# Performance work log

Hardware: AMD Instinct MI355X
Metric: run time of the kernel (lower is better)

The kernel has to match this reference:

```python
import jax, jax.numpy as jnp
import numpy as np
from math import sqrt

N_IN = 1024
N_OUT = 1024
DEPTH = 10
N_NODES = 2 ** (DEPTH + 1) - 1  # 2047
BATCH = 32768


def setup_inputs() -> dict:
    key = jax.random.key(0)
    k1, k2, k3 = jax.random.split(key, 3)
    f1 = 1.0 / sqrt(N_IN)
    f2 = 1.0 / sqrt(DEPTH + 1)
    x = jax.random.normal(k1, (BATCH, N_IN), dtype=jnp.float32)
    w1s = jax.random.uniform(k2, (N_NODES, N_IN), dtype=jnp.float32, minval=-f1, maxval=f1)
    w2s = jax.random.uniform(k3, (N_NODES, N_OUT), dtype=jnp.float32, minval=-f2, maxval=f2)
    return {"x": x, "w1s": w1s, "w2s": w2s, "depth": DEPTH}


def reference(x, w1s, w2s, depth):
    batch = x.shape[0]

    def step(current_node, _):
        # current_node: [b] int32 node index at this tree level
        plane_score = jnp.einsum('bi,bi->b', x, w1s[current_node])  # [b]
        plane_choice = (plane_score > 0).astype(jnp.int32)
        next_node = current_node * 2 + plane_choice + 1
        return next_node, (current_node, plane_score)

    node0 = jnp.zeros((batch,), dtype=jnp.int32)
    _, (all_nodes, all_scores) = jax.lax.scan(step, node0, None, length=depth + 1)
    all_nodes = all_nodes.T    # [b, depth+1]
    all_scores = all_scores.T  # [b, depth+1]

    selected_w2s = w2s[all_nodes]  # [b, depth+1, nOut]
    y = jnp.einsum('bij,bi->bj', selected_w2s, all_scores)
    return y
```

## Files before the change

### kernel.cpp

```cpp
#include <hip/hip_runtime.h>


typedef float        f32x4 __attribute__((ext_vector_type(4)));
typedef unsigned int u32x4 __attribute__((ext_vector_type(4)));

#define FFF_BATCH  32768
#define FFF_NIN    1024
#define FFF_NOUT   1024
#define FFF_LEVELS 11
#define FFF_NODES  2047
#define FFF_EPS    0.02f

__device__ __forceinline__ f32x4 ld_nt4f(const f32x4* p) { return __builtin_nontemporal_load(p); }
__device__ __forceinline__ float ub(unsigned d, int k) {
    return (float)((d >> (8 * k)) & 0xffu);
}

__global__ void fff_quant_u8(const float* __restrict__ w1, const float* __restrict__ w2,
                             unsigned char* __restrict__ q1, unsigned char* __restrict__ q2,
                             float* __restrict__ s1, float* __restrict__ s2)
{
    const int node = blockIdx.x;
    const int t    = threadIdx.x;
    const int wave = t >> 6;
    const int lane = t & 63;

    const f32x4* r1 = reinterpret_cast<const f32x4*>(w1 + (size_t)node * FFF_NIN);
    const f32x4* r2 = reinterpret_cast<const f32x4*>(w2 + (size_t)node * FFF_NOUT);
    const int si = 64 * (t & 3) + (t >> 2);
    const f32x4 v1 = r1[si];
    const f32x4 v2 = r2[si];

    float m1 = 0.f, m2 = 0.f;
#pragma unroll
    for (int k = 0; k < 4; ++k) {
        m1 = fmaxf(m1, fabsf(v1[k]));
        m2 = fmaxf(m2, fabsf(v2[k]));
    }
#pragma unroll
    for (int m = 1; m < 64; m <<= 1) {
        m1 = fmaxf(m1, __shfl_xor(m1, m, 64));
        m2 = fmaxf(m2, __shfl_xor(m2, m, 64));
    }
    __shared__ float sm1[4], sm2[4];
    if (lane == 0) { sm1[wave] = m1; sm2[wave] = m2; }
    __syncthreads();
    m1 = fmaxf(fmaxf(sm1[0], sm1[1]), fmaxf(sm1[2], sm1[3]));
    m2 = fmaxf(fmaxf(sm2[0], sm2[1]), fmaxf(sm2[2], sm2[3]));

    const float st1 = (m1 > 0.f) ? m1 / 127.f : 1.f;
    const float st2 = (m2 > 0.f) ? m2 / 127.f : 1.f;
    if (t == 0) { s1[node] = st1; s2[node] = st2; }

    unsigned d1 = 0, d2 = 0;
#pragma unroll
    for (int k = 0; k < 4; ++k) {
        const int u1 = (int)rintf(v1[k] / st1) + 128;
        const int u2 = (int)rintf(v2[k] / st2) + 128;
        d1 |= ((unsigned)u1 & 0xffu) << (8 * k);
        d2 |= ((unsigned)u2 & 0xffu) << (8 * k);
    }
    reinterpret_cast<unsigned*>(q1)[(size_t)node * 256 + t] = d1;
    reinterpret_cast<unsigned*>(q2)[(size_t)node * 256 + t] = d2;
}

__global__ __launch_bounds__(256, 4) void fff_main_u8(
    const float*         __restrict__ x,
    const unsigned char* __restrict__ q1,
    const float*         __restrict__ s1,
    const float*         __restrict__ w1f,
    const unsigned char* __restrict__ q2,
    const float*         __restrict__ s2,
    float*               __restrict__ y)
{
    const int row  = blockIdx.x * 4 + (threadIdx.x >> 6);
    const int lane = threadIdx.x & 63;

    const f32x4* x4 = reinterpret_cast<const f32x4*>(x + (size_t)row * FFF_NIN);
    f32x4 xv[4];
#pragma unroll
    for (int c = 0; c < 4; ++c) xv[c] = ld_nt4f(&x4[c * 64 + lane]);

    float sumx = 0.f;
#pragma unroll
    for (int c = 0; c < 4; ++c) {
        sumx += xv[c][0]; sumx += xv[c][1]; sumx += xv[c][2]; sumx += xv[c][3];
    }
#pragma unroll
    for (int m = 1; m < 64; m <<= 1) sumx += __shfl_xor(sumx, m, 64);

    f32x4 acc[4];
#pragma unroll
    for (int c = 0; c < 4; ++c) acc[c] = (f32x4)(0.f);
    float corr = 0.f;

    int node = 0;

#pragma unroll 1
    for (int l = 0; l < FFF_LEVELS; ++l) {
        const int un = __builtin_amdgcn_readfirstlane(node);

        const u32x4 d1 = *reinterpret_cast<const u32x4*>(q1 + (size_t)un * 1024 + lane * 16);
        const u32x4 d2 = *reinterpret_cast<const u32x4*>(q2 + (size_t)un * 1024 + lane * 16);
        const float sc1 = s1[un];
        const float sc2 = s2[un];

        float pu = 0.f;
#pragma unroll
        for (int c = 0; c < 4; ++c) {
#pragma unroll
            for (int k = 0; k < 4; ++k)
                pu = fmaf(xv[c][k], ub(d1[c], k), pu);
        }
#pragma unroll
        for (int m = 1; m < 64; m <<= 1) pu += __shfl_xor(pu, m, 64);

        float p = (pu - 128.f * sumx) * sc1;

        if (__builtin_expect(fabsf(p) < FFF_EPS, 0)) {
            const f32x4* w14 = reinterpret_cast<const f32x4*>(w1f + (size_t)un * FFF_NIN);
            float s = 0.f;
#pragma unroll
            for (int c = 0; c < 4; ++c) {
                const f32x4 w = w14[c * 64 + lane];
                s = fmaf(xv[c][0], w[0], s);
                s = fmaf(xv[c][1], w[1], s);
                s = fmaf(xv[c][2], w[2], s);
                s = fmaf(xv[c][3], w[3], s);
            }
#pragma unroll
            for (int m = 1; m < 64; m <<= 1) s += __shfl_xor(s, m, 64);
            p = s;
        }

        const float s2l = p * sc2;
        corr = fmaf(s2l, 128.f, corr);
#pragma unroll
        for (int c = 0; c < 4; ++c) {
#pragma unroll
            for (int k = 0; k < 4; ++k)
                acc[c][k] = fmaf(s2l, ub(d2[c], k), acc[c][k]);
        }

        node = node * 2 + 1 + ((p > 0.f) ? 1 : 0);
    }

    f32x4* y4 = reinterpret_cast<f32x4*>(y + (size_t)row * FFF_NOUT);
#pragma unroll
    for (int c = 0; c < 4; ++c) {
        f32x4 o;
        o[0] = acc[c][0] - corr; o[1] = acc[c][1] - corr;
        o[2] = acc[c][2] - corr; o[3] = acc[c][3] - corr;
        y4[c * 64 + lane] = o;
    }
}

__global__ __launch_bounds__(256, 4) void fff_fused_f32(
    const float* __restrict__ x, const float* __restrict__ w1s,
    const float* __restrict__ w2s, float* __restrict__ y)
{
    const int row  = blockIdx.x * 4 + (threadIdx.x >> 6);
    const int lane = threadIdx.x & 63;
    const f32x4* x4 = reinterpret_cast<const f32x4*>(x + (size_t)row * FFF_NIN);
    f32x4 xv[4];
#pragma unroll
    for (int c = 0; c < 4; ++c) xv[c] = x4[c * 64 + lane];
    f32x4 acc[4];
#pragma unroll
    for (int c = 0; c < 4; ++c) acc[c] = (f32x4)(0.f);
    int node = 0;
#pragma unroll 1
    for (int l = 0; l < FFF_LEVELS; ++l) {
        const f32x4* w14 = reinterpret_cast<const f32x4*>(w1s + (size_t)node * FFF_NIN);
        const f32x4* w24 = reinterpret_cast<const f32x4*>(w2s + (size_t)node * FFF_NOUT);
        f32x4 wv[4], uv[4];
#pragma unroll
        for (int c = 0; c < 4; ++c) { wv[c] = w14[c * 64 + lane]; uv[c] = w24[c * 64 + lane]; }
        float p = 0.f;
#pragma unroll
        for (int c = 0; c < 4; ++c) {
            p = fmaf(xv[c][0], wv[c][0], p); p = fmaf(xv[c][1], wv[c][1], p);
            p = fmaf(xv[c][2], wv[c][2], p); p = fmaf(xv[c][3], wv[c][3], p);
        }
#pragma unroll
        for (int m = 1; m < 64; m <<= 1) p += __shfl_xor(p, m, 64);
#pragma unroll
        for (int c = 0; c < 4; ++c) {
            acc[c][0] = fmaf(p, uv[c][0], acc[c][0]); acc[c][1] = fmaf(p, uv[c][1], acc[c][1]);
            acc[c][2] = fmaf(p, uv[c][2], acc[c][2]); acc[c][3] = fmaf(p, uv[c][3], acc[c][3]);
        }
        node = node * 2 + 1 + ((p > 0.f) ? 1 : 0);
    }
    f32x4* y4 = reinterpret_cast<f32x4*>(y + (size_t)row * FFF_NOUT);
#pragma unroll
    for (int c = 0; c < 4; ++c) y4[c * 64 + lane] = acc[c];
}

extern "C" void kernel_launch(void* const* d_in, const int* in_sizes, int n_in,
                              void* d_out, int out_size, void* d_ws, size_t ws_size,
                              hipStream_t stream) {
    const float* x   = (const float*)d_in[0];
    const float* w1s = (const float*)d_in[1];
    const float* w2s = (const float*)d_in[2];
    float* y = (float*)d_out;

    const size_t sc_bytes = 8192;
    const size_t q_bytes  = (size_t)FFF_NODES * 1024;
    const size_t need = 2 * sc_bytes + 2 * q_bytes;

    if (ws_size >= need) {
        float* s1 = (float*)d_ws;
        float* s2 = (float*)((char*)d_ws + sc_bytes);
        unsigned char* q1 = (unsigned char*)d_ws + 2 * sc_bytes;
        unsigned char* q2 = q1 + q_bytes;
        fff_quant_u8<<<FFF_NODES, 256, 0, stream>>>(w1s, w2s, q1, q2, s1, s2);
        fff_main_u8<<<FFF_BATCH / 4, 256, 0, stream>>>(x, q1, s1, w1s, q2, s2, y);
    } else {
        fff_fused_f32<<<FFF_BATCH / 4, 256, 0, stream>>>(x, w1s, w2s, y);
    }
}
```

Baseline: 85.50 us.

## Prefetch both child nodes' weights speculatively and use DPP wave reductions

Each tree level now issues loads for both possible children's quantized w1/w2 rows and scales before the current level's reduction finishes, then selects the correct one once the branch direction is known. This hides the dependent global-load latency of the tree walk but doubles the weight traffic per level. The shuffle-based butterfly reductions are also replaced with DPP row operations plus a readlane, which should reduce the latency of each cross-lane sum.

Result: slower. 100.5 us (+17.5%).

```diff
diff --git a/kernel.cpp b/kernel.cpp
--- a/kernel.cpp
+++ b/kernel.cpp
@@ -14,6 +14,21 @@
 __device__ __forceinline__ f32x4 ld_nt4f(const f32x4* p) { return __builtin_nontemporal_load(p); }
 __device__ __forceinline__ float ub(unsigned d, int k) {
     return (float)((d >> (8 * k)) & 0xffu);
+}
+
+template<int CTRL>
+__device__ __forceinline__ float dpp_add(float v) {
+    const int t = __builtin_amdgcn_update_dpp(0, __float_as_int(v), CTRL, 0xF, 0xF, true);
+    return v + __int_as_float(t);
+}
+__device__ __forceinline__ float wave_sum(float v) {
+    v = dpp_add<0x111>(v);
+    v = dpp_add<0x112>(v);
+    v = dpp_add<0x114>(v);
+    v = dpp_add<0x118>(v);
+    v = dpp_add<0x142>(v);
+    v = dpp_add<0x143>(v);
+    return __int_as_float(__builtin_amdgcn_readlane(__float_as_int(v), 63));
 }
 
 __global__ void fff_quant_u8(const float* __restrict__ w1, const float* __restrict__ w2,
@@ -81,30 +96,27 @@
 #pragma unroll
     for (int c = 0; c < 4; ++c) xv[c] = ld_nt4f(&x4[c * 64 + lane]);
 
-    float sumx = 0.f;
-#pragma unroll
-    for (int c = 0; c < 4; ++c) {
-        sumx += xv[c][0]; sumx += xv[c][1]; sumx += xv[c][2]; sumx += xv[c][3];
-    }
-#pragma unroll
-    for (int m = 1; m < 64; m <<= 1) sumx += __shfl_xor(sumx, m, 64);
+    float sx = 0.f;
+#pragma unroll
+    for (int c = 0; c < 4; ++c) { sx += xv[c][0]; sx += xv[c][1]; sx += xv[c][2]; sx += xv[c][3]; }
+    const float sumx = wave_sum(sx);
 
     f32x4 acc[4];
 #pragma unroll
     for (int c = 0; c < 4; ++c) acc[c] = (f32x4)(0.f);
     float corr = 0.f;
 
+    const u32x4* q1v = reinterpret_cast<const u32x4*>(q1);
+    const u32x4* q2v = reinterpret_cast<const u32x4*>(q2);
+
     int node = 0;
+    u32x4 d1 = q1v[lane];
+    u32x4 d2 = q2v[lane];
+    float sc1 = s1[0];
+    float sc2 = s2[0];
 
 #pragma unroll 1
     for (int l = 0; l < FFF_LEVELS; ++l) {
-        const int un = __builtin_amdgcn_readfirstlane(node);
-
-        const u32x4 d1 = *reinterpret_cast<const u32x4*>(q1 + (size_t)un * 1024 + lane * 16);
-        const u32x4 d2 = *reinterpret_cast<const u32x4*>(q2 + (size_t)un * 1024 + lane * 16);
-        const float sc1 = s1[un];
-        const float sc2 = s2[un];
-
         float pu = 0.f;
 #pragma unroll
         for (int c = 0; c < 4; ++c) {
@@ -112,13 +124,24 @@
             for (int k = 0; k < 4; ++k)
                 pu = fmaf(xv[c][k], ub(d1[c], k), pu);
         }
-#pragma unroll
-        for (int m = 1; m < 64; m <<= 1) pu += __shfl_xor(pu, m, 64);
-
-        float p = (pu - 128.f * sumx) * sc1;
+
+        const bool has = (l < FFF_LEVELS - 1);
+        u32x4 d1L, d1R, d2L, d2R;
+        float s1L = 0.f, s1R = 0.f, s2L = 0.f, s2R = 0.f;
+        if (has) {
+            const int left = __builtin_amdgcn_readfirstlane(2 * node + 1);
+            d1L = q1v[(size_t)left * 64 + lane];
+            d1R = q1v[(size_t)(left + 1) * 64 + lane];
+            d2L = q2v[(size_t)left * 64 + lane];
+            d2R = q2v[(size_t)(left + 1) * 64 + lane];
+            s1L = s1[left]; s1R = s1[left + 1];
+            s2L = s2[left]; s2R = s2[left + 1];
+        }
+
+        float p = (wave_sum(pu) - 128.f * sumx) * sc1;
 
         if (__builtin_expect(fabsf(p) < FFF_EPS, 0)) {
-            const f32x4* w14 = reinterpret_cast<const f32x4*>(w1f + (size_t)un * FFF_NIN);
+            const f32x4* w14 = reinterpret_cast<const f32x4*>(w1f + (size_t)node * FFF_NIN);
             float s = 0.f;
 #pragma unroll
             for (int c = 0; c < 4; ++c) {
@@ -128,9 +151,7 @@
                 s = fmaf(xv[c][2], w[2], s);
                 s = fmaf(xv[c][3], w[3], s);
             }
-#pragma unroll
-            for (int m = 1; m < 64; m <<= 1) s += __shfl_xor(s, m, 64);
-            p = s;
+            p = wave_sum(s);
         }
 
         const float s2l = p * sc2;
@@ -142,7 +163,14 @@
                 acc[c][k] = fmaf(s2l, ub(d2[c], k), acc[c][k]);
         }
 
-        node = node * 2 + 1 + ((p > 0.f) ? 1 : 0);
+        const bool right = (p > 0.f);
+        node = 2 * node + 1 + (right ? 1 : 0);
+        if (has) {
+            d1  = right ? d1R : d1L;
+            d2  = right ? d2R : d2L;
+            sc1 = right ? s1R : s1L;
+            sc2 = right ? s2R : s2L;
+        }
     }
 
     f32x4* y4 = reinterpret_cast<f32x4*>(y + (size_t)row * FFF_NOUT);
```
